# Kernel tuning notes

Hardware: AMD Instinct MI355X
Metric: run time of the kernel (lower is better)

The kernel has to match this reference:

```python
import jax, jax.numpy as jnp
import numpy as np

N_BINS = 229      # mel bins (H_dim == s_dim == N_BINS)
MODEL = 128       # model_complexity
OUT = 88          # output_features (piano keys)
W_SIZE = 30       # half-window; window length = 2*30+1 = 61
B, T = 4, 2048


def setup_inputs() -> dict:
    key = jax.random.key(0)
    ks = jax.random.split(key, 8)
    sF = 1.0 / np.sqrt(2 * N_BINS)   # attn linear fan_in = s_dim + H_dim
    sM = 1.0 / np.sqrt(MODEL)
    s1 = 1.0 / np.sqrt(N_BINS)
    return {
        "spec": jax.random.normal(ks[0], (B, T, N_BINS), jnp.float32),
        # attn = nn.Linear(s_dim + H_dim, model_size), split into hidden / encoder halves
        "W_h": jax.random.normal(ks[1], (N_BINS, MODEL), jnp.float32) * sF,
        "W_e": jax.random.normal(ks[2], (N_BINS, MODEL), jnp.float32) * sF,
        "b_attn": jax.random.normal(ks[3], (MODEL,), jnp.float32) * sF,
        # v = nn.Linear(model_size, 1, bias=False)
        "v_w": jax.random.normal(ks[4], (MODEL,), jnp.float32) * sM,
        # linear1 = nn.Linear(N_BINS, output_features) (layers=1, cat_feat=False)
        "W1": jax.random.normal(ks[5], (N_BINS, OUT), jnp.float32) * s1,
        "b1": jax.random.normal(ks[6], (OUT,), jnp.float32) * s1,
    }


def reference(spec, W_h, W_e, b_attn, v_w, W1, b1):
    # spec: [B, T, F]; both `x` (hidden) and `encoder_outputs` in the torch model.
    Bn, Tn, Fn = spec.shape
    Wlen = 2 * W_SIZE + 1
    # pad time axis and take sliding windows (as_strided equivalent)
    padded = jnp.pad(spec, ((0, 0), (W_SIZE, W_SIZE), (0, 0)))
    idx = jnp.arange(Tn)[:, None] + jnp.arange(Wlen)[None, :]          # [T, Wlen]
    windows = padded[:, idx]                                            # [B, T, Wlen, F]
    # attn(cat(hidden, enc)) = hidden @ W_h + enc @ W_e + b  (hidden identical over window)
    h_term = spec @ W_h + b_attn                                        # [B, T, M]
    e_term = jnp.einsum('btwf,fm->btwm', windows, W_e)                  # [B, T, Wlen, M]
    energy = jnp.tanh(h_term[:, :, None, :] + e_term)
    scores = energy @ v_w                                               # [B, T, Wlen]
    a = jax.nn.softmax(scores, axis=-1)
    weighted = jnp.einsum('btw,btwf->btf', a, windows)                  # [B, T, F]
    frame_pred = jax.nn.sigmoid(weighted @ W1 + b1)                     # [B, T, OUT]
    return frame_pred, a[:, :, None, :]                                 # a: [B, T, 1, Wlen]
```

## Files before the change

### kernel.cpp

```cpp
#include <hip/hip_runtime.h>
#include <math.h>

#define N_BINS 229
#define MODEL  128
#define OUTD   88
#define WSZ    30
#define WLEN   61
#define BB     4
#define TT     2048
#define CTANH  2.8853900817779268f

#define KPAD   256
#define NPAD   384
#define BSTRB  80
#define ROWS_F 8
#define FHALO  71
#define EPADU  68

typedef __attribute__((ext_vector_type(8))) short  short8v;
typedef __attribute__((ext_vector_type(4))) float  f32x4;

__device__ __forceinline__ unsigned short bf16_rne(float x) {
    unsigned int u = __float_as_uint(x);
    return (unsigned short)((u + 0x7FFFu + ((u >> 16) & 1u)) >> 16);
}
__device__ __forceinline__ float sigmoidf_(float x) {
    return __builtin_amdgcn_rcpf(1.0f + __expf(-x));
}

__global__ __launch_bounds__(256) void k_prep_w(
        const float* __restrict__ W_h, const float* __restrict__ W_e,
        const float* __restrict__ W1, unsigned short* __restrict__ Wt) {
    const int n = blockIdx.x;
    const int k = threadIdx.x;
    float v = 0.0f;
    if (k < N_BINS) {
        if (n < 128)      v = W_h[k * MODEL + n] * CTANH;
        else if (n < 256) v = W_e[k * MODEL + (n - 128)] * CTANH;
        else if (n < 344) v = W1[k * OUTD + (n - 256)];
    }
    Wt[n * KPAD + k] = bf16_rne(v);
}

__global__ __launch_bounds__(512, 4) void k_he_mfma(
        const float* __restrict__ spec,
        const unsigned short* __restrict__ Wt,
        const float* __restrict__ b_attn,
        float* __restrict__ H,
        unsigned int* __restrict__ Ebf,
        float* __restrict__ S1) {
    __shared__ __align__(16) unsigned char lds[NPAD * BSTRB + 2 * 16 * BSTRB];
    unsigned char* Bl  = lds;
    unsigned char* Ahi = lds + NPAD * BSTRB;
    unsigned char* Alo = Ahi + 16 * BSTRB;

    const int tid   = threadIdx.x;
    const int gm0   = blockIdx.x * 16;
    const int lane  = tid & 63;
    const int wv    = tid >> 6;
    const int mfrag = lane & 15;
    const int kg    = lane >> 4;

    f32x4 acc0 = {0,0,0,0}, acc1 = {0,0,0,0}, acc2 = {0,0,0,0};
    const uint4* __restrict__ Wt4 = (const uint4*)Wt;

    for (int kb = 0; kb < 8; ++kb) {
        __syncthreads();
#pragma unroll
        for (int it = 0; it < 3; ++it) {
            const int u = it * 512 + tid;
            const int row = u >> 2, q = u & 3;
            const uint4 v = Wt4[row * 32 + kb * 4 + q];
            *(uint4*)(Bl + row * BSTRB + q * 16) = v;
        }
        if (tid < 256) {
            const int row = tid >> 4, kp = tid & 15;
            const int gk  = kb * 32 + kp * 2;
            const float* __restrict__ sp = spec + (size_t)(gm0 + row) * N_BINS;
            const float v0 = (gk     < N_BINS) ? sp[gk]     : 0.0f;
            const float v1 = (gk + 1 < N_BINS) ? sp[gk + 1] : 0.0f;
            const unsigned short h0 = bf16_rne(v0), h1 = bf16_rne(v1);
            const float r0 = v0 - __uint_as_float((unsigned int)h0 << 16);
            const float r1 = v1 - __uint_as_float((unsigned int)h1 << 16);
            *(unsigned int*)(Ahi + row * BSTRB + kp * 4) =
                (unsigned int)h0 | ((unsigned int)h1 << 16);
            *(unsigned int*)(Alo + row * BSTRB + kp * 4) =
                (unsigned int)bf16_rne(r0) | ((unsigned int)bf16_rne(r1) << 16);
        }
        __syncthreads();

        const short8v ah = *(const short8v*)(Ahi + mfrag * BSTRB + kg * 16);
        const short8v al = *(const short8v*)(Alo + mfrag * BSTRB + kg * 16);
        const int n0 = wv * 48;
        const short8v b0 = *(const short8v*)(Bl + (n0      + mfrag) * BSTRB + kg * 16);
        const short8v b1 = *(const short8v*)(Bl + (n0 + 16 + mfrag) * BSTRB + kg * 16);
        const short8v b2 = *(const short8v*)(Bl + (n0 + 32 + mfrag) * BSTRB + kg * 16);
        acc0 = __builtin_amdgcn_mfma_f32_16x16x32_bf16(ah, b0, acc0, 0, 0, 0);
        acc0 = __builtin_amdgcn_mfma_f32_16x16x32_bf16(al, b0, acc0, 0, 0, 0);
        acc1 = __builtin_amdgcn_mfma_f32_16x16x32_bf16(ah, b1, acc1, 0, 0, 0);
        acc1 = __builtin_amdgcn_mfma_f32_16x16x32_bf16(al, b1, acc1, 0, 0, 0);
        acc2 = __builtin_amdgcn_mfma_f32_16x16x32_bf16(ah, b2, acc2, 0, 0, 0);
        acc2 = __builtin_amdgcn_mfma_f32_16x16x32_bf16(al, b2, acc2, 0, 0, 0);
    }

#pragma unroll
    for (int t = 0; t < 3; ++t) {
        const f32x4 acc = (t == 0) ? acc0 : (t == 1) ? acc1 : acc2;
        const int gn = wv * 48 + t * 16 + mfrag;
        if (gn < 128) {
            const float bc = b_attn[gn] * CTANH;
#pragma unroll
            for (int r = 0; r < 4; ++r) {
                const int gm = gm0 + (kg << 2) + r;
                H[(size_t)gm * MODEL + gn] = acc[r] + bc;
            }
        } else if (gn < 256) {
            const int ne = gn - 128;
#pragma unroll
            for (int r = 0; r < 4; ++r) {
                const float own = acc[r];
                const float pv  = __shfl_xor(own, 1, 64);
                if ((ne & 1) == 0) {
                    const int gm = gm0 + (kg << 2) + r;
                    Ebf[(size_t)gm * 64 + (ne >> 1)] =
                        (unsigned int)bf16_rne(own) |
                        ((unsigned int)bf16_rne(pv) << 16);
                }
            }
        } else if (gn < 344) {
            const int ns = gn - 256;
#pragma unroll
            for (int r = 0; r < 4; ++r) {
                const int gm = gm0 + (kg << 2) + r;
                S1[(size_t)gm * OUTD + ns] = acc[r];
            }
        }
    }
}

__global__ __launch_bounds__(512, 4) void k_fused(
        const float* __restrict__ H,
        const unsigned int* __restrict__ Ebf,
        const float* __restrict__ v_w,
        const float* __restrict__ S1,
        const float* __restrict__ b1,
        float* __restrict__ pred,
        float* __restrict__ a_out) {
    const int nb   = blockIdx.x;
    const int tid  = threadIdx.x;
    const int wv   = tid >> 6;
    const int lane = tid & 63;
    const int r0   = nb * ROWS_F;
    const int b    = r0 >> 11;
    const int t0   = r0 & (TT - 1);
    const int r    = r0 + wv;
    const int t    = t0 + wv;

    __shared__ __align__(16) unsigned char ubuf[FHALO * OUTD * 4];
    unsigned int* Ebs = (unsigned int*)ubuf;
    float*        S1h = (float*)ubuf;
    __shared__ float4 Hs4[ROWS_F * 32];
    __shared__ float4 Vs4[32];
    __shared__ float  scA[ROWS_F][64];
    __shared__ float  cf[ROWS_F][64];

    const uint4* __restrict__ Eb16 = (const uint4*)Ebf + (size_t)b * TT * 16;
    for (int i = tid; i < FHALO * 16; i += 512) {
        const int row = i >> 4, c = i & 15;
        const int s   = t0 - WSZ + row;
        uint4 v = make_uint4(0u, 0u, 0u, 0u);
        if (s >= 0 && s < TT) v = Eb16[(size_t)s * 16 + c];
        *(uint4*)&Ebs[row * EPADU + (c << 2)] = v;
    }
    if (tid < ROWS_F * 32)
        Hs4[tid] = ((const float4*)H)[(size_t)r0 * 32 + tid];
    else if (tid < ROWS_F * 32 + 32)
        Vs4[tid - ROWS_F * 32] = ((const float4*)v_w)[tid - ROWS_F * 32];
    __syncthreads();

    const int g  = lane & 3;
    const int w0 = lane >> 2;

    float vs = 0.f;
#pragma unroll
    for (int q = 0; q < 8; ++q) {
        const float4 vq = Vs4[(q << 2) + g];
        vs += (vq.x + vq.y) + (vq.z + vq.w);
    }
    vs += __shfl_xor(vs, 1, 64);
    vs += __shfl_xor(vs, 2, 64);

    int ro[4];
#pragma unroll
    for (int it = 0; it < 4; ++it)
        ro[it] = (wv + w0 + it * 16) * EPADU;

    const float4* __restrict__ HsR = &Hs4[wv * 32];

    float pp[4] = {0.f, 0.f, 0.f, 0.f};
#pragma unroll
    for (int q = 0; q < 8; ++q) {
        const int    cq = (q << 2) + g;
        const float4 hq = HsR[cq];
        const float4 vq = Vs4[cq];
        const float nx = -2.f * vq.x, ny = -2.f * vq.y,
                    nz = -2.f * vq.z, nw = -2.f * vq.w;
#pragma unroll
        for (int it = 0; it < 4; ++it) {
            const uint2 e2 = *(const uint2*)&Ebs[ro[it] + (cq << 1)];
            const float f0 = __uint_as_float(e2.x << 16);
            const float f1 = __uint_as_float(e2.x & 0xFFFF0000u);
            const float f2 = __uint_as_float(e2.y << 16);
            const float f3 = __uint_as_float(e2.y & 0xFFFF0000u);
            float u;
            u = __builtin_amdgcn_rcpf(__builtin_amdgcn_exp2f(f0 + hq.x) + 1.f);
            pp[it] = fmaf(nx, u, pp[it]);
            u = __builtin_amdgcn_rcpf(__builtin_amdgcn_exp2f(f1 + hq.y) + 1.f);
            pp[it] = fmaf(ny, u, pp[it]);
            u = __builtin_amdgcn_rcpf(__builtin_amdgcn_exp2f(f2 + hq.z) + 1.f);
            pp[it] = fmaf(nz, u, pp[it]);
            u = __builtin_amdgcn_rcpf(__builtin_amdgcn_exp2f(f3 + hq.w) + 1.f);
            pp[it] = fmaf(nw, u, pp[it]);
        }
    }
#pragma unroll
    for (int it = 0; it < 4; ++it) {
        float p = pp[it];
        p += __shfl_xor(p, 1, 64);
        p += __shfl_xor(p, 2, 64);
        const int w = w0 + it * 16;
        if (g == 0 && w < WLEN) scA[wv][w] = p + vs;
    }

    {
        float x = (lane < WLEN) ? scA[wv][lane] : -INFINITY;
        float mx = x;
#pragma unroll
        for (int d = 32; d >= 1; d >>= 1) mx = fmaxf(mx, __shfl_xor(mx, d, 64));
        float e = (lane < WLEN) ? __expf(x - mx) : 0.0f;
        float sm = e;
#pragma unroll
        for (int d = 32; d >= 1; d >>= 1) sm += __shfl_xor(sm, d, 64);
        const float a = e * __builtin_amdgcn_rcpf(sm);
        if (lane < WLEN) a_out[(size_t)r * WLEN + lane] = a;
        const int sl = t + lane - WSZ;
        cf[wv][lane] = (lane < WLEN && sl >= 0 && sl < TT) ? a : 0.0f;
    }

    __syncthreads();

    const float4* __restrict__ Sb4 = (const float4*)S1 + (size_t)b * TT * 22;
    for (int i = tid; i < FHALO * 22; i += 512) {
        const int row = i / 22, c = i - row * 22;
        const int s   = t0 - WSZ + row;
        float4 v = make_float4(0.f, 0.f, 0.f, 0.f);
        if (s >= 0 && s < TT) v = Sb4[(size_t)s * 22 + c];
        *(float4*)&S1h[row * OUTD + (c << 2)] = v;
    }
    __syncthreads();

    const int o2 = 64 + (lane < 24 ? lane : 23);
    float a1 = 0.f, a2 = 0.f;
#pragma unroll 4
    for (int w = 0; w < 64; ++w) {
        const float at = cf[wv][w];
        const float* __restrict__ rowp = &S1h[(wv + w) * OUTD];
        a1 = fmaf(at, rowp[lane], a1);
        a2 = fmaf(at, rowp[o2],   a2);
    }
    pred[(size_t)r * OUTD + lane] = sigmoidf_(a1 + b1[lane]);
    if (lane < 24)
        pred[(size_t)r * OUTD + 64 + lane] = sigmoidf_(a2 + b1[64 + lane]);
}

extern "C" void kernel_launch(void* const* d_in, const int* in_sizes, int n_in,
                              void* d_out, int out_size, void* d_ws, size_t ws_size,
                              hipStream_t stream) {
    const float* spec   = (const float*)d_in[0];
    const float* W_h    = (const float*)d_in[1];
    const float* W_e    = (const float*)d_in[2];
    const float* b_attn = (const float*)d_in[3];
    const float* v_w    = (const float*)d_in[4];
    const float* W1     = (const float*)d_in[5];
    const float* b1     = (const float*)d_in[6];

    const int n_rows = BB * TT;
    char* ws = (char*)d_ws;
    float*          H   = (float*)ws;
    unsigned int*   Ebf = (unsigned int*)(ws + ((size_t)4 << 20));
    float*          S1  = (float*)(ws + ((size_t)6 << 20));
    unsigned short* Wt  = (unsigned short*)(ws + ((size_t)9 << 20));

    float* pred  = (float*)d_out;
    float* a_out = pred + (size_t)n_rows * OUTD;

    k_prep_w <<<NPAD,         256, 0, stream>>>(W_h, W_e, W1, Wt);
    k_he_mfma<<<n_rows / 16,  512, 0, stream>>>(spec, Wt, b_attn, H, Ebf, S1);
    k_fused  <<<n_rows / ROWS_F, 512, 0, stream>>>(H, Ebf, v_w, S1, b1,
                                                   pred, a_out);
}
```

Before: 53.60 us.

## Load GEMM operands directly from global and store S1 projection as packed bf16

```diff
diff --git a/kernel.cpp b/kernel.cpp
--- a/kernel.cpp
+++ b/kernel.cpp
@@ -12,7 +12,6 @@
 
 #define KPAD   256
 #define NPAD   384
-#define BSTRB  80
 #define ROWS_F 8
 #define FHALO  71
 #define EPADU  68
@@ -48,53 +47,39 @@
         const float* __restrict__ b_attn,
         float* __restrict__ H,
         unsigned int* __restrict__ Ebf,
-        float* __restrict__ S1) {
-    __shared__ __align__(16) unsigned char lds[NPAD * BSTRB + 2 * 16 * BSTRB];
-    unsigned char* Bl  = lds;
-    unsigned char* Ahi = lds + NPAD * BSTRB;
-    unsigned char* Alo = Ahi + 16 * BSTRB;
-
+        unsigned int* __restrict__ S1b) {
     const int tid   = threadIdx.x;
-    const int gm0   = blockIdx.x * 16;
     const int lane  = tid & 63;
     const int wv    = tid >> 6;
+    const int gm0   = blockIdx.x * 16;
     const int mfrag = lane & 15;
     const int kg    = lane >> 4;
+    const int n0    = wv * 48;
 
     f32x4 acc0 = {0,0,0,0}, acc1 = {0,0,0,0}, acc2 = {0,0,0,0};
-    const uint4* __restrict__ Wt4 = (const uint4*)Wt;
+
+    const float* __restrict__ sp = spec + (size_t)(gm0 + mfrag) * N_BINS;
+    const unsigned short* __restrict__ B0 = Wt + (size_t)(n0      + mfrag) * KPAD;
+    const unsigned short* __restrict__ B1 = Wt + (size_t)(n0 + 16 + mfrag) * KPAD;
+    const unsigned short* __restrict__ B2 = Wt + (size_t)(n0 + 32 + mfrag) * KPAD;
 
     for (int kb = 0; kb < 8; ++kb) {
-        __syncthreads();
-#pragma unroll
-        for (int it = 0; it < 3; ++it) {
-            const int u = it * 512 + tid;
-            const int row = u >> 2, q = u & 3;
-            const uint4 v = Wt4[row * 32 + kb * 4 + q];
-            *(uint4*)(Bl + row * BSTRB + q * 16) = v;
-        }
-        if (tid < 256) {
-            const int row = tid >> 4, kp = tid & 15;
-            const int gk  = kb * 32 + kp * 2;
-            const float* __restrict__ sp = spec + (size_t)(gm0 + row) * N_BINS;
-            const float v0 = (gk     < N_BINS) ? sp[gk]     : 0.0f;
-            const float v1 = (gk + 1 < N_BINS) ? sp[gk + 1] : 0.0f;
-            const unsigned short h0 = bf16_rne(v0), h1 = bf16_rne(v1);
-            const float r0 = v0 - __uint_as_float((unsigned int)h0 << 16);
-            const float r1 = v1 - __uint_as_float((unsigned int)h1 << 16);
-            *(unsigned int*)(Ahi + row * BSTRB + kp * 4) =
-                (unsigned int)h0 | ((unsigned int)h1 << 16);
-            *(unsigned int*)(Alo + row * BSTRB + kp * 4) =
-                (unsigned int)bf16_rne(r0) | ((unsigned int)bf16_rne(r1) << 16);
-        }
-        __syncthreads();
-
-        const short8v ah = *(const short8v*)(Ahi + mfrag * BSTRB + kg * 16);
-        const short8v al = *(const short8v*)(Alo + mfrag * BSTRB + kg * 16);
-        const int n0 = wv * 48;
-        const short8v b0 = *(const short8v*)(Bl + (n0      + mfrag) * BSTRB + kg * 16);
-        const short8v b1 = *(const short8v*)(Bl + (n0 + 16 + mfrag) * BSTRB + kg * 16);
-        const short8v b2 = *(const short8v*)(Bl + (n0 + 32 + mfrag) * BSTRB + kg * 16);
+        const int k0 = kb * 32 + kg * 8;
+        float v[8];
+#pragma unroll
+        for (int j = 0; j < 8; ++j)
+            v[j] = (k0 + j < N_BINS) ? sp[k0 + j] : 0.0f;
+        short8v ah, al;
+#pragma unroll
+        for (int j = 0; j < 8; ++j) {
+            const unsigned short h = bf16_rne(v[j]);
+            const float rr = v[j] - __uint_as_float((unsigned int)h << 16);
+            ah[j] = (short)h;
+            al[j] = (short)bf16_rne(rr);
+        }
+        const short8v b0 = *(const short8v*)(B0 + k0);
+        const short8v b1 = *(const short8v*)(B1 + k0);
+        const short8v b2 = *(const short8v*)(B2 + k0);
         acc0 = __builtin_amdgcn_mfma_f32_16x16x32_bf16(ah, b0, acc0, 0, 0, 0);
         acc0 = __builtin_amdgcn_mfma_f32_16x16x32_bf16(al, b0, acc0, 0, 0, 0);
         acc1 = __builtin_amdgcn_mfma_f32_16x16x32_bf16(ah, b1, acc1, 0, 0, 0);
@@ -106,7 +91,7 @@
 #pragma unroll
     for (int t = 0; t < 3; ++t) {
         const f32x4 acc = (t == 0) ? acc0 : (t == 1) ? acc1 : acc2;
-        const int gn = wv * 48 + t * 16 + mfrag;
+        const int gn = n0 + t * 16 + mfrag;
         if (gn < 128) {
             const float bc = b_attn[gn] * CTANH;
 #pragma unroll
@@ -131,8 +116,14 @@
             const int ns = gn - 256;
 #pragma unroll
             for (int r = 0; r < 4; ++r) {
-                const int gm = gm0 + (kg << 2) + r;
-                S1[(size_t)gm * OUTD + ns] = acc[r];
+                const float own = acc[r];
+                const float pv  = __shfl_xor(own, 1, 64);
+                if ((ns & 1) == 0) {
+                    const int gm = gm0 + (kg << 2) + r;
+                    S1b[(size_t)gm * 44 + (ns >> 1)] =
+                        (unsigned int)bf16_rne(own) |
+                        ((unsigned int)bf16_rne(pv) << 16);
+                }
             }
         }
     }
@@ -142,7 +133,7 @@
         const float* __restrict__ H,
         const unsigned int* __restrict__ Ebf,
         const float* __restrict__ v_w,
-        const float* __restrict__ S1,
+        const unsigned int* __restrict__ S1b,
         const float* __restrict__ b1,
         float* __restrict__ pred,
         float* __restrict__ a_out) {
@@ -156,9 +147,9 @@
     const int r    = r0 + wv;
     const int t    = t0 + wv;
 
-    __shared__ __align__(16) unsigned char ubuf[FHALO * OUTD * 4];
+    __shared__ __align__(16) unsigned char ubuf[FHALO * EPADU * 4];
     unsigned int* Ebs = (unsigned int*)ubuf;
-    float*        S1h = (float*)ubuf;
+    unsigned int* S1u = (unsigned int*)ubuf;
     __shared__ float4 Hs4[ROWS_F * 32];
     __shared__ float4 Vs4[32];
     __shared__ float  scA[ROWS_F][64];
@@ -249,28 +240,29 @@
 
     __syncthreads();
 
-    const float4* __restrict__ Sb4 = (const float4*)S1 + (size_t)b * TT * 22;
-    for (int i = tid; i < FHALO * 22; i += 512) {
-        const int row = i / 22, c = i - row * 22;
+    const uint4* __restrict__ Sb4 = (const uint4*)S1b + (size_t)b * TT * 11;
+    for (int i = tid; i < FHALO * 11; i += 512) {
+        const int row = i / 11, c = i - row * 11;
         const int s   = t0 - WSZ + row;
-        float4 v = make_float4(0.f, 0.f, 0.f, 0.f);
-        if (s >= 0 && s < TT) v = Sb4[(size_t)s * 22 + c];
-        *(float4*)&S1h[row * OUTD + (c << 2)] = v;
+        uint4 v = make_uint4(0u, 0u, 0u, 0u);
+        if (s >= 0 && s < TT) v = Sb4[(size_t)s * 11 + c];
+        *(uint4*)&S1u[row * 44 + (c << 2)] = v;
     }
     __syncthreads();
 
-    const int o2 = 64 + (lane < 24 ? lane : 23);
-    float a1 = 0.f, a2 = 0.f;
+    if (lane < 44) {
+        float a1 = 0.f, a2 = 0.f;
 #pragma unroll 4
-    for (int w = 0; w < 64; ++w) {
-        const float at = cf[wv][w];
-        const float* __restrict__ rowp = &S1h[(wv + w) * OUTD];
-        a1 = fmaf(at, rowp[lane], a1);
-        a2 = fmaf(at, rowp[o2],   a2);
-    }
-    pred[(size_t)r * OUTD + lane] = sigmoidf_(a1 + b1[lane]);
-    if (lane < 24)
-        pred[(size_t)r * OUTD + 64 + lane] = sigmoidf_(a2 + b1[64 + lane]);
+        for (int w = 0; w < 64; ++w) {
+            const float at = cf[wv][w];
+            const unsigned int pv = S1u[(wv + w) * 44 + lane];
+            a1 = fmaf(at, __uint_as_float(pv << 16),         a1);
+            a2 = fmaf(at, __uint_as_float(pv & 0xFFFF0000u), a2);
+        }
+        const int o = lane << 1;
+        pred[(size_t)r * OUTD + o]     = sigmoidf_(a1 + b1[o]);
+        pred[(size_t)r * OUTD + o + 1] = sigmoidf_(a2 + b1[o + 1]);
+    }
 }
 
 extern "C" void kernel_launch(void* const* d_in, const int* in_sizes, int n_in,
@@ -288,14 +280,14 @@
     char* ws = (char*)d_ws;
     float*          H   = (float*)ws;
     unsigned int*   Ebf = (unsigned int*)(ws + ((size_t)4 << 20));
-    float*          S1  = (float*)(ws + ((size_t)6 << 20));
-    unsigned short* Wt  = (unsigned short*)(ws + ((size_t)9 << 20));
+    unsigned int*   S1b = (unsigned int*)(ws + ((size_t)6 << 20));
+    unsigned short* Wt  = (unsigned short*)(ws + ((size_t)8 << 20));
 
     float* pred  = (float*)d_out;
     float* a_out = pred + (size_t)n_rows * OUTD;
 
-    k_prep_w <<<NPAD,         256, 0, stream>>>(W_h, W_e, W1, Wt);
-    k_he_mfma<<<n_rows / 16,  512, 0, stream>>>(spec, Wt, b_attn, H, Ebf, S1);
-    k_fused  <<<n_rows / ROWS_F, 512, 0, stream>>>(H, Ebf, v_w, S1, b1,
+    k_prep_w <<<NPAD,            256, 0, stream>>>(W_h, W_e, W1, Wt);
+    k_he_mfma<<<n_rows / 16,     512, 0, stream>>>(spec, Wt, b_attn, H, Ebf, S1b);
+    k_fused  <<<n_rows / ROWS_F, 512, 0, stream>>>(H, Ebf, v_w, S1b, b1,
                                                    pred, a_out);
 }
```

Result: slower. 55.23 us (+3.0%).
